# Optimization experiments

Measured on AMD Instinct MI355X. Metric: run time of the kernel, lower is better.

The kernel has to match this reference:

```python
import jax, jax.numpy as jnp
import numpy as np

B, L, D, H = 2, 1024, 1024, 16
Dh = D // H


def setup_inputs() -> dict:
    key = jax.random.key(0)
    ks = jax.random.split(key, 11)
    w_scale = 1.0 / np.sqrt(D).astype(np.float32)
    def w(k):
        return jax.random.normal(k, (D, D), dtype=jnp.float32) * w_scale
    def b(k):
        return jax.random.normal(k, (D,), dtype=jnp.float32) * 0.01
    return {
        "x": jax.random.normal(ks[0], (B, L, D), dtype=jnp.float32),
        "Wq": w(ks[1]), "bq": b(ks[2]),
        "Wk1": w(ks[3]), "bk1": b(ks[4]),
        "Wv": w(ks[5]), "bv": b(ks[6]),
        "Wk2": w(ks[7]), "bk2": b(ks[8]),
        "Wp": w(ks[9]), "bp": b(ks[10]),
    }


def reference(x, Wq, bq, Wk1, bk1, Wv, bv, Wk2, bk2, Wp, bp):
    Bx, Lx, Dx = x.shape
    lin = lambda t, W, b_: t @ W + b_
    # AR branch: kernelized accumulation of K^T V
    Q = lin(x, Wq, bq).reshape(Bx, Lx, H, Dh)      # (B,L,H,Dh)
    K = lin(x, Wk1, bk1).reshape(Bx, Lx, H, Dh)
    V = lin(x, Wv, bv).reshape(Bx, Lx, H, Dh)
    Wacc = jnp.cumsum(jnp.einsum('blhd,blhe->blhde', K, V), axis=1)  # (B,L,H,Dh,Dh)
    O1 = jnp.einsum('blhd,blhde->blhe', Q, Wacc)   # (B,L,H,Dh)
    # MA branch on one-step residuals
    V_raw = x.reshape(Bx, Lx, H, Dh)
    E = V_raw[:, 1:] - O1[:, :-1]                  # (B,L-1,H,Dh)
    z = lin(x[:, :-1], Wk2, bk2) / jnp.sqrt(jnp.float32(Dx))
    k2 = jax.nn.sigmoid(z * 0.02).reshape(Bx, Lx - 1, H, Dh)
    q2 = -jax.nn.leaky_relu(-Q[:, :-1] / jnp.sqrt(jnp.float32(Dh)), negative_slope=0.02)
    WE = jnp.cumsum(jnp.einsum('blhd,blhe->blhde', k2, E), axis=1)  # (B,L-1,H,Dh,Dh)
    O2 = jnp.einsum('blhd,blhde->blhe', q2, WE)
    O2 = jnp.concatenate([jnp.zeros_like(O2[:, :1]), O2], axis=1)   # (B,L,H,Dh)
    y = (O1 + O2).reshape(Bx, Lx, Dx)
    return lin(y, Wp, bp)
```

## Files before the change

### kernel.cpp

```cpp
#include <hip/hip_runtime.h>
#include <hip/hip_bf16.h>
#include <math.h>

#define Bsz 2
#define Lsz 1024
#define Dsz 1024
#define Hsz 16
#define Dh 64
#define Mtot (Bsz*Lsz)
#define NC (Lsz/64)
#define LPAD 72

typedef __bf16 bf16_t;
typedef bf16_t bf16x8 __attribute__((ext_vector_type(8)));
typedef bf16_t bf16x4 __attribute__((ext_vector_type(4)));
typedef float f32x4v __attribute__((ext_vector_type(4)));

__device__ __forceinline__ void gload16(const void* g, void* l) {
    __builtin_amdgcn_global_load_lds(
        (const __attribute__((address_space(1))) unsigned int*)g,
        (__attribute__((address_space(3))) unsigned int*)l, 16, 0, 0);
}

template<int MODE>
__global__ __launch_bounds__(256) void bgemm_kernel(
    const bf16_t* __restrict__ A, const bf16_t* __restrict__ Bt,
    const float* b0, const float* b1, const float* b2, const float* b3,
    bf16_t* Qo, bf16_t* q2o, bf16_t* Ko, bf16_t* Vo, bf16_t* k2o, float* Cout)
{
    constexpr int TM   = (MODE == 0) ? 128 : 64;
    constexpr int MF   = (MODE == 0) ? 4 : 2;
    constexpr int L    = (MODE == 0) ? 4 : 3;
    constexpr int ASZ  = TM * 32;

    __shared__ __align__(16) bf16_t As[3][ASZ];
    __shared__ __align__(16) bf16_t Bs[3][4096];
    const int tid  = threadIdx.x;
    const int lane = tid & 63;
    const int wid  = tid >> 6;

    const int lin = blockIdx.x;
    const int xcd = lin & 7;
    const int t0  = lin >> 3;
    int brow, bcolg;
    if (MODE == 0) {
        brow  = (xcd & 1) * 8 + (t0 & 7);
        bcolg = (xcd >> 1) * 8 + (t0 >> 3);
    } else {
        brow  = (xcd & 3) * 8 + (t0 & 7);
        bcolg = (xcd >> 2) * 4 + (t0 >> 3);
    }
    const int row0  = brow * TM;
    const int col0g = bcolg * 128;
    const int p    = col0g >> 10;
    const int col0 = col0g & 1023;
    const int wr = (wid >> 1) * (TM / 2);
    const int wc = (wid & 1) * 64;

    const int srow = tid >> 2;
    const int scol = tid & 3;
    const int ssw  = (srow & 3) ^ ((srow >> 2) & 3);
    const int scol_sw = scol ^ ssw;
    const bf16_t* gA0 = A  + (size_t)(row0 + srow)       * 1024 + scol_sw * 8;
    const bf16_t* gA1 = A  + (size_t)(row0 + srow + 64)  * 1024 + scol_sw * 8;
    const bf16_t* gB0 = Bt + (size_t)(col0g + srow)      * 1024 + scol_sw * 8;
    const bf16_t* gB1 = Bt + (size_t)(col0g + srow + 64) * 1024 + scol_sw * 8;

    const int laneRow = lane & 15;
    const int kblk = lane >> 4;
    const int swz = (kblk ^ (laneRow & 3) ^ ((laneRow >> 2) & 3)) & 3;
    const int aoff = (wr + laneRow) * 32 + swz * 8;
    const int boff = (wc + laneRow) * 32 + swz * 8;

    f32x4v acc[MF][4];
    #pragma unroll
    for (int i = 0; i < MF; ++i)
        #pragma unroll
        for (int j = 0; j < 4; ++j)
            acc[i][j] = (f32x4v){0.f, 0.f, 0.f, 0.f};

    auto stage = [&](int buf) {
        gload16(gA0, &As[buf][tid * 8]);
        if (MODE == 0) gload16(gA1, &As[buf][(tid + 256) * 8]);
        gload16(gB0, &Bs[buf][tid * 8]);
        gload16(gB1, &Bs[buf][(tid + 256) * 8]);
        gA0 += 32; gA1 += 32; gB0 += 32; gB1 += 32;
    };

    stage(0); stage(1);
    if (MODE == 0) { asm volatile("s_waitcnt vmcnt(4)" ::: "memory"); }
    else           { asm volatile("s_waitcnt vmcnt(3)" ::: "memory"); }
    __builtin_amdgcn_s_barrier();

    int cur = 0;
    for (int t = 0; t < 32; ++t) {
        bf16x8 af[MF], bfr[4];
        #pragma unroll
        for (int f = 0; f < MF; ++f)
            af[f]  = *reinterpret_cast<const bf16x8*>(&As[cur][aoff + f * 512]);
        #pragma unroll
        for (int f = 0; f < 4; ++f)
            bfr[f] = *reinterpret_cast<const bf16x8*>(&Bs[cur][boff + f * 512]);
        if (t < 30) {
            int nxt = cur + 2; if (nxt >= 3) nxt -= 3;
            stage(nxt);
        }
        #pragma unroll
        for (int i = 0; i < MF; ++i)
            #pragma unroll
            for (int j = 0; j < 4; ++j)
                acc[i][j] = __builtin_amdgcn_mfma_f32_16x16x32_bf16(af[i], bfr[j], acc[i][j], 0, 0, 0);
        if (t < 30) {
            if (MODE == 0) { asm volatile("s_waitcnt vmcnt(4)" ::: "memory"); }
            else           { asm volatile("s_waitcnt vmcnt(3)" ::: "memory"); }
        } else if (t == 30) {
            asm volatile("s_waitcnt vmcnt(0)" ::: "memory");
        }
        if (t < 31) __builtin_amdgcn_s_barrier();
        cur = (cur == 2) ? 0 : cur + 1;
    }

    const int crowb = row0 + wr + kblk * 4;
    const int ccolb = col0 + wc + laneRow;
    const float* bias = (MODE == 1) ? b0 : (p == 0) ? b0 : (p == 1) ? b1 : (p == 2) ? b2 : b3;
    float bv[4];
    #pragma unroll
    for (int j = 0; j < 4; ++j) bv[j] = bias[ccolb + j * 16];
    #pragma unroll
    for (int i = 0; i < MF; ++i)
        #pragma unroll
        for (int j = 0; j < 4; ++j)
            #pragma unroll
            for (int e = 0; e < 4; ++e) {
                const float val = acc[i][j][e] + bv[j];
                const size_t idx = (size_t)(crowb + i * 16 + e) * 1024 + ccolb + j * 16;
                if (MODE == 1) {
                    Cout[idx] = val;
                } else if (p == 0) {
                    Qo[idx]  = (bf16_t)val;
                    q2o[idx] = (bf16_t)((val >= 0.f ? 0.02f * val : val) * 0.125f);
                } else if (p == 1) {
                    Ko[idx] = (bf16_t)val;
                } else if (p == 2) {
                    Vo[idx] = (bf16_t)val;
                } else {
                    k2o[idx] = (bf16_t)(1.f / (1.f + __expf(-val * 0.000625f)));
                }
            }
}

__global__ __launch_bounds__(256) void prep_kernel(
    const float* __restrict__ x, bf16_t* __restrict__ xb,
    const float* __restrict__ W0, const float* __restrict__ W1,
    const float* __restrict__ W2, const float* __restrict__ W3,
    const float* __restrict__ W4, bf16_t* __restrict__ Wt)
{
    const int z = blockIdx.z;
    const int tid = threadIdx.x;
    if (z == 5) {
        const int lin = blockIdx.y * 16 + blockIdx.x;
        #pragma unroll
        for (int u = 0; u < 8; ++u) {
            const size_t s = (size_t)lin * 2048 + u * 256 + tid;
            float4 v = *reinterpret_cast<const float4*>(&x[s * 4]);
            bf16x4 o;
            o[0] = (bf16_t)v.x; o[1] = (bf16_t)v.y; o[2] = (bf16_t)v.z; o[3] = (bf16_t)v.w;
            *reinterpret_cast<bf16x4*>(&xb[s * 4]) = o;
        }
        return;
    }
    const float* W = (z == 0) ? W0 : (z == 1) ? W1 : (z == 2) ? W2 : (z == 3) ? W3 : W4;
    bf16_t* T = Wt + (size_t)z * 1048576;

    __shared__ float Ls[64][65];
    const int k0 = blockIdx.x * 64;
    const int n0 = blockIdx.y * 64;
    const int r  = tid >> 4;
    const int c4 = (tid & 15) * 4;
    #pragma unroll
    for (int i = 0; i < 4; ++i) {
        float4 v = *reinterpret_cast<const float4*>(&W[(size_t)(k0 + r + i * 16) * Dsz + n0 + c4]);
        Ls[r + i * 16][c4 + 0] = v.x;
        Ls[r + i * 16][c4 + 1] = v.y;
        Ls[r + i * 16][c4 + 2] = v.z;
        Ls[r + i * 16][c4 + 3] = v.w;
    }
    __syncthreads();
    #pragma unroll
    for (int i = 0; i < 4; ++i) {
        const int n = r + i * 16;
        bf16x4 o;
        o[0] = (bf16_t)Ls[c4 + 0][n];
        o[1] = (bf16_t)Ls[c4 + 1][n];
        o[2] = (bf16_t)Ls[c4 + 2][n];
        o[3] = (bf16_t)Ls[c4 + 3][n];
        *reinterpret_cast<bf16x4*>(&T[(size_t)(n0 + n) * Dsz + k0 + c4]) = o;
    }
}

__global__ __launch_bounds__(256) void chunk_intra_kernel(
    const bf16_t* __restrict__ Ap, const bf16_t* __restrict__ Kp,
    const bf16_t* __restrict__ Vp, bf16_t* __restrict__ Oi, bf16_t* __restrict__ dT)
{
    __shared__ __align__(16) bf16_t sQ[64 * LPAD];
    __shared__ __align__(16) bf16_t sK[64 * LPAD];
    __shared__ __align__(16) bf16_t sKt[64 * LPAD];
    __shared__ __align__(16) bf16_t sVt[64 * LPAD];
    __shared__ __align__(16) bf16_t sP[64 * LPAD];

    const int bid = blockIdx.x;
    const int c  = bid & (NC - 1);
    const int bh = bid >> 4;
    const int b = bh >> 4, h = bh & 15;
    const int tid = threadIdx.x;
    const size_t gbase = ((size_t)b * Lsz + (size_t)c * 64) * Dsz + h * Dh;

    #pragma unroll
    for (int cc = tid; cc < 512; cc += 256) {
        const int j = cc >> 3;
        const int d0 = (cc & 7) * 8;
        const size_t g = gbase + (size_t)j * 1024 + d0;
        bf16x8 qv = *reinterpret_cast<const bf16x8*>(&Ap[g]);
        bf16x8 kv = *reinterpret_cast<const bf16x8*>(&Kp[g]);
        bf16x8 vv = *reinterpret_cast<const bf16x8*>(&Vp[g]);
        *reinterpret_cast<bf16x8*>(&sQ[j * LPAD + d0]) = qv;
        *reinterpret_cast<bf16x8*>(&sK[j * LPAD + d0]) = kv;
        #pragma unroll
        for (int i = 0; i < 8; ++i) {
            sKt[(d0 + i) * LPAD + j] = kv[i];
            sVt[(d0 + i) * LPAD + j] = vv[i];
        }
    }
    __syncthreads();

    const int w = tid >> 6;
    const int lane = tid & 63;
    const int lr = lane & 15;
    const int kb = lane >> 4;
    const int m0 = w * 16;

    f32x4v accp[4], acct[4];
    #pragma unroll
    for (int n = 0; n < 4; ++n) { accp[n] = (f32x4v){0,0,0,0}; acct[n] = (f32x4v){0,0,0,0}; }
    #pragma unroll
    for (int kk = 0; kk < 2; ++kk) {
        const int c0 = kk * 32 + kb * 8;
        bf16x8 aq = *reinterpret_cast<const bf16x8*>(&sQ [(m0 + lr) * LPAD + c0]);
        bf16x8 av = *reinterpret_cast<const bf16x8*>(&sVt[(m0 + lr) * LPAD + c0]);
        #pragma unroll
        for (int n = 0; n < 4; ++n) {
            bf16x8 bk = *reinterpret_cast<const bf16x8*>(&sK [(n * 16 + lr) * LPAD + c0]);
            bf16x8 bt = *reinterpret_cast<const bf16x8*>(&sKt[(n * 16 + lr) * LPAD + c0]);
            accp[n] = __builtin_amdgcn_mfma_f32_16x16x32_bf16(aq, bk, accp[n], 0, 0, 0);
            acct[n] = __builtin_amdgcn_mfma_f32_16x16x32_bf16(av, bt, acct[n], 0, 0, 0);
        }
    }

    const size_t tbase = (size_t)bid * 4096;
    #pragma unroll
    for (int n = 0; n < 4; ++n)
        #pragma unroll
        for (int e = 0; e < 4; ++e) {
            const int r = m0 + kb * 4 + e;
            const int col = n * 16 + lr;
            dT[tbase + (size_t)r * 64 + col] = (bf16_t)acct[n][e];
            sP[r * LPAD + col] = (bf16_t)((col <= r) ? accp[n][e] : 0.f);
        }
    __syncthreads();

    f32x4v acco[4];
    #pragma unroll
    for (int n = 0; n < 4; ++n) acco[n] = (f32x4v){0,0,0,0};
    #pragma unroll
    for (int kk = 0; kk < 2; ++kk) {
        const int c0 = kk * 32 + kb * 8;
        bf16x8 a = *reinterpret_cast<const bf16x8*>(&sP[(m0 + lr) * LPAD + c0]);
        #pragma unroll
        for (int n = 0; n < 4; ++n) {
            bf16x8 bb = *reinterpret_cast<const bf16x8*>(&sVt[(n * 16 + lr) * LPAD + c0]);
            acco[n] = __builtin_amdgcn_mfma_f32_16x16x32_bf16(a, bb, acco[n], 0, 0, 0);
        }
    }
    #pragma unroll
    for (int n = 0; n < 4; ++n)
        #pragma unroll
        for (int e = 0; e < 4; ++e)
            Oi[gbase + (size_t)(m0 + kb * 4 + e) * 1024 + n * 16 + lr] = (bf16_t)acco[n][e];
}

__global__ __launch_bounds__(256) void inter1_intra2_kernel(
    const bf16_t* __restrict__ Qr, const bf16_t* __restrict__ q2p,
    const bf16_t* __restrict__ k2p, const bf16_t* __restrict__ dT1,
    const bf16_t* __restrict__ Oi1, const float* __restrict__ x,
    float* __restrict__ O1g, bf16_t* __restrict__ dT2, bf16_t* __restrict__ Oi2)
{
    __shared__ __align__(16) bf16_t sQ  [64 * LPAD];
    __shared__ __align__(16) bf16_t sq2 [64 * LPAD];
    __shared__ __align__(16) bf16_t sK2 [64 * LPAD];
    __shared__ __align__(16) bf16_t sk2t[64 * LPAD];
    __shared__ __align__(16) bf16_t sEt [64 * LPAD];
    __shared__ __align__(16) bf16_t sP  [64 * LPAD];
    __shared__ __align__(16) bf16_t sT  [64 * LPAD];

    const int bid = blockIdx.x;
    const int c  = bid & (NC - 1);
    const int bh = bid >> 4;
    const int b = bh >> 4, h = bh & 15;
    const int tid = threadIdx.x;
    const size_t gbase = ((size_t)b * Lsz + (size_t)c * 64) * Dsz + h * Dh;

    #pragma unroll
    for (int it = 0; it < 2; ++it) {
        const int cc = tid + it * 256;
        const int j = cc >> 3;
        const int d0 = (cc & 7) * 8;
        const size_t g = gbase + (size_t)j * 1024 + d0;
        bf16x8 qv  = *reinterpret_cast<const bf16x8*>(&Qr[g]);
        bf16x8 q2v = *reinterpret_cast<const bf16x8*>(&q2p[g]);
        bf16x8 k2v = *reinterpret_cast<const bf16x8*>(&k2p[g]);
        *reinterpret_cast<bf16x8*>(&sQ [j * LPAD + d0]) = qv;
        *reinterpret_cast<bf16x8*>(&sq2[j * LPAD + d0]) = q2v;
        *reinterpret_cast<bf16x8*>(&sK2[j * LPAD + d0]) = k2v;
        #pragma unroll
        for (int i = 0; i < 8; ++i)
            sk2t[(d0 + i) * LPAD + j] = k2v[i];
    }
    {
        const bf16_t* tb = dT1 + (size_t)bh * NC * 4096 + tid * 16;
        float acc[16];
        #pragma unroll
        for (int k = 0; k < 16; ++k) acc[k] = 0.f;
        for (int cc = 0; cc < c; ++cc) {
            bf16x8 v0 = *reinterpret_cast<const bf16x8*>(&tb[(size_t)cc * 4096]);
            bf16x8 v1 = *reinterpret_cast<const bf16x8*>(&tb[(size_t)cc * 4096 + 8]);
            #pragma unroll
            for (int k = 0; k < 8; ++k) { acc[k] += (float)v0[k]; acc[8 + k] += (float)v1[k]; }
        }
        const int row = tid >> 2;
        const int c16 = (tid & 3) * 16;
        bf16x8 o0, o1v;
        #pragma unroll
        for (int k = 0; k < 8; ++k) { o0[k] = (bf16_t)acc[k]; o1v[k] = (bf16_t)acc[8 + k]; }
        *reinterpret_cast<bf16x8*>(&sT[row * LPAD + c16]) = o0;
        *reinterpret_cast<bf16x8*>(&sT[row * LPAD + c16 + 8]) = o1v;
    }
    __syncthreads();

    const int w = tid >> 6;
    const int lane = tid & 63;
    const int lr = lane & 15;
    const int kb = lane >> 4;
    const int m0 = w * 16;

    f32x4v acci[4], accp[4];
    #pragma unroll
    for (int n = 0; n < 4; ++n) { acci[n] = (f32x4v){0,0,0,0}; accp[n] = (f32x4v){0,0,0,0}; }
    #pragma unroll
    for (int kk = 0; kk < 2; ++kk) {
        const int c0 = kk * 32 + kb * 8;
        bf16x8 aq  = *reinterpret_cast<const bf16x8*>(&sQ [(m0 + lr) * LPAD + c0]);
        bf16x8 aq2 = *reinterpret_cast<const bf16x8*>(&sq2[(m0 + lr) * LPAD + c0]);
        #pragma unroll
        for (int n = 0; n < 4; ++n) {
            bf16x8 bs = *reinterpret_cast<const bf16x8*>(&sT [(n * 16 + lr) * LPAD + c0]);
            bf16x8 bk = *reinterpret_cast<const bf16x8*>(&sK2[(n * 16 + lr) * LPAD + c0]);
            acci[n] = __builtin_amdgcn_mfma_f32_16x16x32_bf16(aq,  bs, acci[n], 0, 0, 0);
            accp[n] = __builtin_amdgcn_mfma_f32_16x16x32_bf16(aq2, bk, accp[n], 0, 0, 0);
        }
    }
    #pragma unroll
    for (int n = 0; n < 4; ++n)
        #pragma unroll
        for (int e = 0; e < 4; ++e) {
            const int iLoc = m0 + kb * 4 + e;
            const int col = n * 16 + lr;
            const int lg = c * 64 + iLoc;
            const size_t idx = gbase + (size_t)iLoc * 1024 + col;
            const float o1 = acci[n][e] + (float)Oi1[idx];
            O1g[idx] = o1;
            const float ev = (lg < Lsz - 1) ? (x[idx + 1024] - o1) : 0.f;
            sEt[col * LPAD + iLoc] = (bf16_t)ev;
            sP[iLoc * LPAD + col] = (bf16_t)((col <= iLoc) ? accp[n][e] : 0.f);
        }
    __syncthreads();

    f32x4v acct[4], oi2[4];
    #pragma unroll
    for (int n = 0; n < 4; ++n) { acct[n] = (f32x4v){0,0,0,0}; oi2[n] = (f32x4v){0,0,0,0}; }
    #pragma unroll
    for (int kk = 0; kk < 2; ++kk) {
        const int c0 = kk * 32 + kb * 8;
        bf16x8 ae = *reinterpret_cast<const bf16x8*>(&sEt[(m0 + lr) * LPAD + c0]);
        bf16x8 ap = *reinterpret_cast<const bf16x8*>(&sP [(m0 + lr) * LPAD + c0]);
        #pragma unroll
        for (int n = 0; n < 4; ++n) {
            bf16x8 bt = *reinterpret_cast<const bf16x8*>(&sk2t[(n * 16 + lr) * LPAD + c0]);
            bf16x8 be = *reinterpret_cast<const bf16x8*>(&sEt [(n * 16 + lr) * LPAD + c0]);
            acct[n] = __builtin_amdgcn_mfma_f32_16x16x32_bf16(ae, bt, acct[n], 0, 0, 0);
            oi2[n]  = __builtin_amdgcn_mfma_f32_16x16x32_bf16(ap, be, oi2[n],  0, 0, 0);
        }
    }
    const size_t tbase = (size_t)bid * 4096;
    #pragma unroll
    for (int n = 0; n < 4; ++n)
        #pragma unroll
        for (int e = 0; e < 4; ++e) {
            const int r = m0 + kb * 4 + e;
            const int col = n * 16 + lr;
            dT2[tbase + (size_t)r * 64 + col] = (bf16_t)acct[n][e];
            Oi2[gbase + (size_t)r * 1024 + col] = (bf16_t)oi2[n][e];
        }
}

__global__ __launch_bounds__(256) void inter2_kernel(
    const bf16_t* __restrict__ Ap, const bf16_t* __restrict__ dT,
    const bf16_t* __restrict__ Oi, const float* __restrict__ o1in,
    bf16_t* __restrict__ yb)
{
    __shared__ __align__(16) bf16_t sA[64 * LPAD];
    __shared__ __align__(16) bf16_t sT[64 * LPAD];

    const int bid = blockIdx.x;
    const int c  = bid & (NC - 1);
    const int bh = bid >> 4;
    const int b = bh >> 4, h = bh & 15;
    const int tid = threadIdx.x;
    const size_t gbase = ((size_t)b * Lsz + (size_t)c * 64) * Dsz + h * Dh;

    #pragma unroll
    for (int cc = tid; cc < 512; cc += 256) {
        const int j = cc >> 3;
        const int d0 = (cc & 7) * 8;
        bf16x8 av = *reinterpret_cast<const bf16x8*>(&Ap[gbase + (size_t)j * 1024 + d0]);
        *reinterpret_cast<bf16x8*>(&sA[j * LPAD + d0]) = av;
    }
    {
        const bf16_t* tb = dT + (size_t)bh * NC * 4096 + tid * 16;
        float acc[16];
        #pragma unroll
        for (int k = 0; k < 16; ++k) acc[k] = 0.f;
        for (int cc = 0; cc < c; ++cc) {
            bf16x8 v0 = *reinterpret_cast<const bf16x8*>(&tb[(size_t)cc * 4096]);
            bf16x8 v1 = *reinterpret_cast<const bf16x8*>(&tb[(size_t)cc * 4096 + 8]);
            #pragma unroll
            for (int k = 0; k < 8; ++k) { acc[k] += (float)v0[k]; acc[8 + k] += (float)v1[k]; }
        }
        const int row = tid >> 2;
        const int c16 = (tid & 3) * 16;
        bf16x8 o0, o1v;
        #pragma unroll
        for (int k = 0; k < 8; ++k) { o0[k] = (bf16_t)acc[k]; o1v[k] = (bf16_t)acc[8 + k]; }
        *reinterpret_cast<bf16x8*>(&sT[row * LPAD + c16]) = o0;
        *reinterpret_cast<bf16x8*>(&sT[row * LPAD + c16 + 8]) = o1v;
    }
    __syncthreads();

    const int w = tid >> 6;
    const int lane = tid & 63;
    const int lr = lane & 15;
    const int kb = lane >> 4;
    const int m0 = w * 16;

    f32x4v acc[4];
    #pragma unroll
    for (int n = 0; n < 4; ++n) acc[n] = (f32x4v){0,0,0,0};
    #pragma unroll
    for (int kk = 0; kk < 2; ++kk) {
        const int c0 = kk * 32 + kb * 8;
        bf16x8 a = *reinterpret_cast<const bf16x8*>(&sA[(m0 + lr) * LPAD + c0]);
        #pragma unroll
        for (int n = 0; n < 4; ++n) {
            bf16x8 bb = *reinterpret_cast<const bf16x8*>(&sT[(n * 16 + lr) * LPAD + c0]);
            acc[n] = __builtin_amdgcn_mfma_f32_16x16x32_bf16(a, bb, acc[n], 0, 0, 0);
        }
    }

    #pragma unroll
    for (int n = 0; n < 4; ++n)
        #pragma unroll
        for (int e = 0; e < 4; ++e) {
            const int iLoc = m0 + kb * 4 + e;
            const int lg = c * 64 + iLoc;
            const size_t idx = gbase + (size_t)iLoc * 1024 + n * 16 + lr;
            const float o2 = acc[n][e] + (float)Oi[idx];
            if (lg < Lsz - 1) yb[idx + 1024] = (bf16_t)(o1in[idx + 1024] + o2);
            if (lg == 0)      yb[idx] = (bf16_t)(o1in[idx]);
        }
}

extern "C" void kernel_launch(void* const* d_in, const int* in_sizes, int n_in,
                              void* d_out, int out_size, void* d_ws, size_t ws_size,
                              hipStream_t stream) {
    const float* x   = (const float*)d_in[0];
    const float* Wq  = (const float*)d_in[1];
    const float* bq  = (const float*)d_in[2];
    const float* Wk1 = (const float*)d_in[3];
    const float* bk1 = (const float*)d_in[4];
    const float* Wv  = (const float*)d_in[5];
    const float* bv  = (const float*)d_in[6];
    const float* Wk2 = (const float*)d_in[7];
    const float* bk2 = (const float*)d_in[8];
    const float* Wp  = (const float*)d_in[9];
    const float* bp  = (const float*)d_in[10];
    float* out = (float*)d_out;
    float* ws  = (float*)d_ws;

    const size_t mat = (size_t)Mtot * Dsz;
    float*  O1  = ws;
    bf16_t* Oib = (bf16_t*)(ws + 2 * mat);
    bf16_t* dT1 = (bf16_t*)(ws + 3 * mat);
    bf16_t* dT2 = (bf16_t*)(ws + 4 * mat);
    bf16_t* xb  = (bf16_t*)(ws + 5 * mat);
    bf16_t* Wt  = (bf16_t*)(ws + 6 * mat);
    float*  bb  = ws + 8 * mat + mat / 2;
    bf16_t* Qr  = (bf16_t*)(bb);
    bf16_t* q2  = (bf16_t*)(bb + mat / 2);
    bf16_t* Kb  = (bf16_t*)(bb + mat);
    bf16_t* Vb  = (bf16_t*)(bb + 3 * mat / 2);
    bf16_t* k2  = (bf16_t*)(bb + 2 * mat);
    bf16_t* yb  = Qr;

    dim3 block(256);

    prep_kernel<<<dim3(16, 16, 6), block, 0, stream>>>(x, xb, Wq, Wk1, Wv, Wk2, Wp, Wt);

    bgemm_kernel<0><<<dim3(512), block, 0, stream>>>(
        xb, Wt, bq, bk1, bv, bk2, Qr, q2, Kb, Vb, k2, nullptr);

    chunk_intra_kernel<<<dim3(512), block, 0, stream>>>(Qr, Kb, Vb, Oib, dT1);
    inter1_intra2_kernel<<<dim3(512), block, 0, stream>>>(Qr, q2, k2, dT1, Oib, x, O1, dT2, Oib);
    inter2_kernel<<<dim3(512), block, 0, stream>>>(q2, dT2, Oib, O1, yb);

    bgemm_kernel<1><<<dim3(256), block, 0, stream>>>(
        yb, Wt + 4 * 1048576, bp, nullptr, nullptr, nullptr,
        nullptr, nullptr, nullptr, nullptr, nullptr, out);
}
```

Baseline: 92.42 us.

## Widen projection GEMM tile to 128x256 and store O1 intermediate in bf16

```diff
diff --git a/kernel.cpp b/kernel.cpp
--- a/kernel.cpp
+++ b/kernel.cpp
@@ -28,13 +28,13 @@
     const float* b0, const float* b1, const float* b2, const float* b3,
     bf16_t* Qo, bf16_t* q2o, bf16_t* Ko, bf16_t* Vo, bf16_t* k2o, float* Cout)
 {
-    constexpr int TM   = (MODE == 0) ? 128 : 64;
-    constexpr int MF   = (MODE == 0) ? 4 : 2;
-    constexpr int L    = (MODE == 0) ? 4 : 3;
-    constexpr int ASZ  = TM * 32;
-
-    __shared__ __align__(16) bf16_t As[3][ASZ];
-    __shared__ __align__(16) bf16_t Bs[3][4096];
+    constexpr int TM = (MODE == 0) ? 128 : 64;
+    constexpr int TN = (MODE == 0) ? 256 : 128;
+    constexpr int MF = (MODE == 0) ? 4 : 2;
+    constexpr int NF = (MODE == 0) ? 8 : 4;
+
+    __shared__ __align__(16) bf16_t As[3][TM * 32];
+    __shared__ __align__(16) bf16_t Bs[3][TN * 32];
     const int tid  = threadIdx.x;
     const int lane = tid & 63;
     const int wid  = tid >> 6;
@@ -45,26 +45,28 @@
     int brow, bcolg;
     if (MODE == 0) {
         brow  = (xcd & 1) * 8 + (t0 & 7);
-        bcolg = (xcd >> 1) * 8 + (t0 >> 3);
+        bcolg = (xcd >> 1) * 4 + (t0 >> 3);
     } else {
         brow  = (xcd & 3) * 8 + (t0 & 7);
         bcolg = (xcd >> 2) * 4 + (t0 >> 3);
     }
     const int row0  = brow * TM;
-    const int col0g = bcolg * 128;
+    const int col0g = bcolg * TN;
     const int p    = col0g >> 10;
     const int col0 = col0g & 1023;
-    const int wr = (wid >> 1) * (TM / 2);
-    const int wc = (wid & 1) * 64;
+    const int wr = (wid >> 1) * (MF * 16);
+    const int wc = (wid & 1) * (NF * 16);
 
     const int srow = tid >> 2;
     const int scol = tid & 3;
     const int ssw  = (srow & 3) ^ ((srow >> 2) & 3);
     const int scol_sw = scol ^ ssw;
-    const bf16_t* gA0 = A  + (size_t)(row0 + srow)       * 1024 + scol_sw * 8;
-    const bf16_t* gA1 = A  + (size_t)(row0 + srow + 64)  * 1024 + scol_sw * 8;
-    const bf16_t* gB0 = Bt + (size_t)(col0g + srow)      * 1024 + scol_sw * 8;
-    const bf16_t* gB1 = Bt + (size_t)(col0g + srow + 64) * 1024 + scol_sw * 8;
+    const bf16_t* gA0 = A  + (size_t)(row0 + srow)        * 1024 + scol_sw * 8;
+    const bf16_t* gA1 = A  + (size_t)(row0 + srow + 64)   * 1024 + scol_sw * 8;
+    const bf16_t* gB0 = Bt + (size_t)(col0g + srow)       * 1024 + scol_sw * 8;
+    const bf16_t* gB1 = Bt + (size_t)(col0g + srow + 64)  * 1024 + scol_sw * 8;
+    const bf16_t* gB2 = Bt + (size_t)(col0g + srow + 128) * 1024 + scol_sw * 8;
+    const bf16_t* gB3 = Bt + (size_t)(col0g + srow + 192) * 1024 + scol_sw * 8;
 
     const int laneRow = lane & 15;
     const int kblk = lane >> 4;
@@ -72,11 +74,11 @@
     const int aoff = (wr + laneRow) * 32 + swz * 8;
     const int boff = (wc + laneRow) * 32 + swz * 8;
 
-    f32x4v acc[MF][4];
+    f32x4v acc[MF][NF];
     #pragma unroll
     for (int i = 0; i < MF; ++i)
         #pragma unroll
-        for (int j = 0; j < 4; ++j)
+        for (int j = 0; j < NF; ++j)
             acc[i][j] = (f32x4v){0.f, 0.f, 0.f, 0.f};
 
     auto stage = [&](int buf) {
@@ -84,22 +86,26 @@
         if (MODE == 0) gload16(gA1, &As[buf][(tid + 256) * 8]);
         gload16(gB0, &Bs[buf][tid * 8]);
         gload16(gB1, &Bs[buf][(tid + 256) * 8]);
-        gA0 += 32; gA1 += 32; gB0 += 32; gB1 += 32;
+        if (MODE == 0) {
+            gload16(gB2, &Bs[buf][(tid + 512) * 8]);
+            gload16(gB3, &Bs[buf][(tid + 768) * 8]);
+        }
+        gA0 += 32; gA1 += 32; gB0 += 32; gB1 += 32; gB2 += 32; gB3 += 32;
     };
 
     stage(0); stage(1);
-    if (MODE == 0) { asm volatile("s_waitcnt vmcnt(4)" ::: "memory"); }
+    if (MODE == 0) { asm volatile("s_waitcnt vmcnt(6)" ::: "memory"); }
     else           { asm volatile("s_waitcnt vmcnt(3)" ::: "memory"); }
     __builtin_amdgcn_s_barrier();
 
     int cur = 0;
     for (int t = 0; t < 32; ++t) {
-        bf16x8 af[MF], bfr[4];
+        bf16x8 af[MF], bfr[NF];
         #pragma unroll
         for (int f = 0; f < MF; ++f)
             af[f]  = *reinterpret_cast<const bf16x8*>(&As[cur][aoff + f * 512]);
         #pragma unroll
-        for (int f = 0; f < 4; ++f)
+        for (int f = 0; f < NF; ++f)
             bfr[f] = *reinterpret_cast<const bf16x8*>(&Bs[cur][boff + f * 512]);
         if (t < 30) {
             int nxt = cur + 2; if (nxt >= 3) nxt -= 3;
@@ -108,10 +114,10 @@
         #pragma unroll
         for (int i = 0; i < MF; ++i)
             #pragma unroll
-            for (int j = 0; j < 4; ++j)
+            for (int j = 0; j < NF; ++j)
                 acc[i][j] = __builtin_amdgcn_mfma_f32_16x16x32_bf16(af[i], bfr[j], acc[i][j], 0, 0, 0);
         if (t < 30) {
-            if (MODE == 0) { asm volatile("s_waitcnt vmcnt(4)" ::: "memory"); }
+            if (MODE == 0) { asm volatile("s_waitcnt vmcnt(6)" ::: "memory"); }
             else           { asm volatile("s_waitcnt vmcnt(3)" ::: "memory"); }
         } else if (t == 30) {
             asm volatile("s_waitcnt vmcnt(0)" ::: "memory");
@@ -123,13 +129,13 @@
     const int crowb = row0 + wr + kblk * 4;
     const int ccolb = col0 + wc + laneRow;
     const float* bias = (MODE == 1) ? b0 : (p == 0) ? b0 : (p == 1) ? b1 : (p == 2) ? b2 : b3;
-    float bv[4];
-    #pragma unroll
-    for (int j = 0; j < 4; ++j) bv[j] = bias[ccolb + j * 16];
+    float bv[NF];
+    #pragma unroll
+    for (int j = 0; j < NF; ++j) bv[j] = bias[ccolb + j * 16];
     #pragma unroll
     for (int i = 0; i < MF; ++i)
         #pragma unroll
-        for (int j = 0; j < 4; ++j)
+        for (int j = 0; j < NF; ++j)
             #pragma unroll
             for (int e = 0; e < 4; ++e) {
                 const float val = acc[i][j][e] + bv[j];
@@ -292,7 +298,7 @@
     const bf16_t* __restrict__ Qr, const bf16_t* __restrict__ q2p,
     const bf16_t* __restrict__ k2p, const bf16_t* __restrict__ dT1,
     const bf16_t* __restrict__ Oi1, const float* __restrict__ x,
-    float* __restrict__ O1g, bf16_t* __restrict__ dT2, bf16_t* __restrict__ Oi2)
+    bf16_t* __restrict__ O1g, bf16_t* __restrict__ dT2, bf16_t* __restrict__ Oi2)
 {
     __shared__ __align__(16) bf16_t sQ  [64 * LPAD];
     __shared__ __align__(16) bf16_t sq2 [64 * LPAD];
@@ -377,7 +383,7 @@
             const int lg = c * 64 + iLoc;
             const size_t idx = gbase + (size_t)iLoc * 1024 + col;
             const float o1 = acci[n][e] + (float)Oi1[idx];
-            O1g[idx] = o1;
+            O1g[idx] = (bf16_t)o1;
             const float ev = (lg < Lsz - 1) ? (x[idx + 1024] - o1) : 0.f;
             sEt[col * LPAD + iLoc] = (bf16_t)ev;
             sP[iLoc * LPAD + col] = (bf16_t)((col <= iLoc) ? accp[n][e] : 0.f);
@@ -414,7 +420,7 @@
 
 __global__ __launch_bounds__(256) void inter2_kernel(
     const bf16_t* __restrict__ Ap, const bf16_t* __restrict__ dT,
-    const bf16_t* __restrict__ Oi, const float* __restrict__ o1in,
+    const bf16_t* __restrict__ Oi, const bf16_t* __restrict__ o1in,
     bf16_t* __restrict__ yb)
 {
     __shared__ __align__(16) bf16_t sA[64 * LPAD];
@@ -483,8 +489,8 @@
             const int lg = c * 64 + iLoc;
             const size_t idx = gbase + (size_t)iLoc * 1024 + n * 16 + lr;
             const float o2 = acc[n][e] + (float)Oi[idx];
-            if (lg < Lsz - 1) yb[idx + 1024] = (bf16_t)(o1in[idx + 1024] + o2);
-            if (lg == 0)      yb[idx] = (bf16_t)(o1in[idx]);
+            if (lg < Lsz - 1) yb[idx + 1024] = (bf16_t)((float)o1in[idx + 1024] + o2);
+            if (lg == 0)      yb[idx] = o1in[idx];
         }
 }
 
@@ -506,7 +512,7 @@
     float* ws  = (float*)d_ws;
 
     const size_t mat = (size_t)Mtot * Dsz;
-    float*  O1  = ws;
+    bf16_t* O1  = (bf16_t*)ws;
     bf16_t* Oib = (bf16_t*)(ws + 2 * mat);
     bf16_t* dT1 = (bf16_t*)(ws + 3 * mat);
     bf16_t* dT2 = (bf16_t*)(ws + 4 * mat);
@@ -524,7 +530,7 @@
 
     prep_kernel<<<dim3(16, 16, 6), block, 0, stream>>>(x, xb, Wq, Wk1, Wv, Wk2, Wp, Wt);
 
-    bgemm_kernel<0><<<dim3(512), block, 0, stream>>>(
+    bgemm_kernel<0><<<dim3(256), block, 0, stream>>>(
         xb, Wt, bq, bk1, bv, bk2, Qr, q2, Kb, Vb, k2, nullptr);
 
     chunk_intra_kernel<<<dim3(512), block, 0, stream>>>(Qr, Kb, Vb, Oib, dT1);
```

Result: slower. 106.6 us (+15.4%).
